# Performance work log

Measured on AMD Instinct MI355X. Metric: run time of the kernel, lower is better.

Reference implementation:

```python
import jax, jax.numpy as jnp
import numpy as np

N = 100000
E_RAND = 1600000
F_IN = 500
HID = 32
N_CLS = 40
EPS = 1e-12


def setup_inputs() -> dict:
    key = jax.random.key(0)
    k_x, k_e, k_w1, k_b1, k_w2, k_b2 = jax.random.split(key, 6)
    x = jax.random.normal(k_x, (N, F_IN), dtype=jnp.float32)
    # random edges (src, dst) + self-loops (PyG AGNNConv adds self-loops)
    er = jax.random.randint(k_e, (2, E_RAND), 0, N, dtype=jnp.int64)
    loops = jnp.broadcast_to(jnp.arange(N, dtype=jnp.int64), (2, N))
    edge_index = jnp.concatenate([er, loops], axis=1)  # [2, 1_700_000]
    W1 = jax.random.normal(k_w1, (F_IN, HID), dtype=jnp.float32) * (1.0 / np.sqrt(F_IN))
    b1 = jax.random.normal(k_b1, (HID,), dtype=jnp.float32) * 0.01
    W2 = jax.random.normal(k_w2, (HID, N_CLS), dtype=jnp.float32) * (1.0 / np.sqrt(HID))
    b2 = jax.random.normal(k_b2, (N_CLS,), dtype=jnp.float32) * 0.01
    beta2 = jnp.float32(1.0)  # learnable beta of prop2
    return {"x": x, "W1": W1, "b1": b1, "W2": W2, "b2": b2,
            "beta2": beta2, "edge_index": edge_index}


def agnn_conv(x, edge_index, beta):
    # x: [N, D]; edge_index: [2, E] with (src=j, dst=i); PyG AGNNConv semantics.
    src, dst = edge_index[0], edge_index[1]
    xn = x * jax.lax.rsqrt(jnp.sum(x * x, axis=-1, keepdims=True) + EPS)  # L2 normalize
    logits = beta * jnp.sum(xn[src] * xn[dst], axis=-1)  # [E] cosine similarity
    # segment softmax over incoming edges of each dst node (self-loops => no empty segments)
    m = jax.ops.segment_max(logits, dst, num_segments=N)
    e = jnp.exp(logits - m[dst])
    s = jax.ops.segment_sum(e, dst, num_segments=N)
    alpha = e / (s[dst] + 1e-16)  # [E]
    out = jax.ops.segment_sum(alpha[:, None] * x[src], dst, num_segments=N)  # [N, D]
    return out


def reference(x, W1, b1, W2, b2, beta2, edge_index):
    # eval mode: dropout is identity
    h = jax.nn.relu(x @ W1 + b1)                 # [N, HID]
    h = agnn_conv(h, edge_index, jnp.float32(1.0))  # prop1: fixed beta
    h = agnn_conv(h, edge_index, beta2)             # prop2: learnable beta
    return h @ W2 + b2                              # [N, N_CLS]
```

## Files before the change

### kernel.cpp

```cpp
#include <hip/hip_runtime.h>
#include <hip/hip_bf16.h>
#include <math.h>

#define F_IN 500
#define HID 32
#define NCLS 40


__global__ void hist_kernel(const int* __restrict__ dst, int E, int* __restrict__ deg) {
    int e = blockIdx.x * 256 + threadIdx.x;
    if (e < E) atomicAdd(&deg[dst[e]], 1);
}

__global__ __launch_bounds__(1024) void scan_local_kernel(const int* __restrict__ deg,
                                                          int* __restrict__ rowptr,
                                                          int* __restrict__ blocksum, int N) {
    __shared__ int wsum[16];
    int tid = threadIdx.x;
    int lane = tid & 63;
    int wid = tid >> 6;
    int idx = blockIdx.x * 1024 + tid;
    int v = (idx < N) ? deg[idx] : 0;
    int x = v;
    #pragma unroll
    for (int off = 1; off < 64; off <<= 1) {
        int y = __shfl_up(x, off);
        if (lane >= off) x += y;
    }
    if (lane == 63) wsum[wid] = x;
    __syncthreads();
    if (wid == 0 && lane < 16) {
        int wv = wsum[lane];
        #pragma unroll
        for (int off = 1; off < 16; off <<= 1) {
            int y = __shfl_up(wv, off);
            if (lane >= off) wv += y;
        }
        wsum[lane] = wv;
    }
    __syncthreads();
    int base = (wid > 0) ? wsum[wid - 1] : 0;
    if (idx < N) rowptr[idx] = base + x - v;
    if (tid == 0) blocksum[blockIdx.x] = wsum[15];
}

__global__ __launch_bounds__(128) void scan_offsets_kernel(int* __restrict__ blocksum,
                                                           int* __restrict__ rowptrN, int nb) {
    __shared__ int ws[2];
    int tid = threadIdx.x;
    int lane = tid & 63;
    int wid = tid >> 6;
    int v = (tid < nb) ? blocksum[tid] : 0;
    int x = v;
    #pragma unroll
    for (int off = 1; off < 64; off <<= 1) {
        int y = __shfl_up(x, off);
        if (lane >= off) x += y;
    }
    if (lane == 63) ws[wid] = x;
    __syncthreads();
    int base = (wid == 1) ? ws[0] : 0;
    int excl = base + x - v;
    if (tid < nb) blocksum[tid] = excl;
    if (tid == nb - 1) *rowptrN = excl + v;
}

__global__ __launch_bounds__(1024) void scan_add_kernel(const int* __restrict__ blocksum,
                                                        int* __restrict__ rowptr,
                                                        int* __restrict__ cursor, int N) {
    int idx = blockIdx.x * 1024 + threadIdx.x;
    if (idx < N) {
        int v = rowptr[idx] + blocksum[blockIdx.x];
        rowptr[idx] = v;
        cursor[idx] = v;
    }
}

__global__ void scatter_kernel(const int* __restrict__ src, const int* __restrict__ dst,
                               int E, int* __restrict__ cursor, int* __restrict__ col) {
    int e = blockIdx.x * 256 + threadIdx.x;
    if (e < E) {
        int pos = atomicAdd(&cursor[dst[e]], 1);
        col[pos] = src[e];
    }
}

__global__ __launch_bounds__(256) void gemm1_kernel(const float* __restrict__ x,
                                                    const float* __restrict__ W1,
                                                    const float* __restrict__ b1,
                                                    float* __restrict__ h1,
                                                    float* __restrict__ rn, int N) {
    __shared__ float xs[128][33];
    __shared__ float w1s[32][32];
    int tid = threadIdx.x;
    int ct = tid & 3;
    int rt = tid >> 2;
    long row0 = (long)blockIdx.x * 128;

    float acc[2][8];
    #pragma unroll
    for (int q = 0; q < 2; ++q)
        #pragma unroll
        for (int j = 0; j < 8; ++j) acc[q][j] = 0.f;

    float4 xr[4];
    float w1r[4];

    #pragma unroll
    for (int s = 0; s < 4; ++s) {
        int f4 = tid + (s << 8);
        int row = f4 >> 3;
        int c4 = (f4 & 7) << 2;
        long gr = row0 + row;
        xr[s] = make_float4(0.f, 0.f, 0.f, 0.f);
        if (gr < N && c4 < F_IN) xr[s] = *(const float4*)(x + gr * F_IN + c4);
        int idx = tid + (s << 8);
        w1r[s] = W1[(long)(idx >> 5) * 32 + (idx & 31)];
    }

    for (int kc = 0; kc < 512; kc += 32) {
        __syncthreads();
        #pragma unroll
        for (int s = 0; s < 4; ++s) {
            int f4 = tid + (s << 8);
            int row = f4 >> 3;
            int c4 = (f4 & 7) << 2;
            xs[row][c4 + 0] = xr[s].x;
            xs[row][c4 + 1] = xr[s].y;
            xs[row][c4 + 2] = xr[s].z;
            xs[row][c4 + 3] = xr[s].w;
            int idx = tid + (s << 8);
            w1s[idx >> 5][idx & 31] = w1r[s];
        }
        __syncthreads();

        int kn = kc + 32;
        if (kn < 512) {
            #pragma unroll
            for (int s = 0; s < 4; ++s) {
                int f4 = tid + (s << 8);
                int row = f4 >> 3;
                int c4 = (f4 & 7) << 2;
                long gr = row0 + row;
                int k = kn + c4;
                xr[s] = make_float4(0.f, 0.f, 0.f, 0.f);
                if (gr < N && k < F_IN) xr[s] = *(const float4*)(x + gr * F_IN + k);
                int idx = tid + (s << 8);
                int kk = kn + (idx >> 5);
                w1r[s] = (kk < F_IN) ? W1[(long)kk * 32 + (idx & 31)] : 0.f;
            }
        }

        #pragma unroll 8
        for (int kk = 0; kk < 32; ++kk) {
            float4 wa = *(const float4*)&w1s[kk][ct * 8];
            float4 wb = *(const float4*)&w1s[kk][ct * 8 + 4];
            float x0 = xs[rt * 2 + 0][kk];
            float x1 = xs[rt * 2 + 1][kk];
            acc[0][0] += x0 * wa.x; acc[0][1] += x0 * wa.y;
            acc[0][2] += x0 * wa.z; acc[0][3] += x0 * wa.w;
            acc[0][4] += x0 * wb.x; acc[0][5] += x0 * wb.y;
            acc[0][6] += x0 * wb.z; acc[0][7] += x0 * wb.w;
            acc[1][0] += x1 * wa.x; acc[1][1] += x1 * wa.y;
            acc[1][2] += x1 * wa.z; acc[1][3] += x1 * wa.w;
            acc[1][4] += x1 * wb.x; acc[1][5] += x1 * wb.y;
            acc[1][6] += x1 * wb.z; acc[1][7] += x1 * wb.w;
        }
    }

    float4 ba = *(const float4*)(b1 + ct * 8);
    float4 bb = *(const float4*)(b1 + ct * 8 + 4);
    #pragma unroll
    for (int q = 0; q < 2; ++q) {
        long gr = row0 + rt * 2 + q;
        float4 oa, ob;
        oa.x = fmaxf(acc[q][0] + ba.x, 0.f);
        oa.y = fmaxf(acc[q][1] + ba.y, 0.f);
        oa.z = fmaxf(acc[q][2] + ba.z, 0.f);
        oa.w = fmaxf(acc[q][3] + ba.w, 0.f);
        ob.x = fmaxf(acc[q][4] + bb.x, 0.f);
        ob.y = fmaxf(acc[q][5] + bb.y, 0.f);
        ob.z = fmaxf(acc[q][6] + bb.z, 0.f);
        ob.w = fmaxf(acc[q][7] + bb.w, 0.f);
        float ss = oa.x * oa.x + oa.y * oa.y + oa.z * oa.z + oa.w * oa.w
                 + ob.x * ob.x + ob.y * ob.y + ob.z * ob.z + ob.w * ob.w;
        ss += __shfl_xor(ss, 1);
        ss += __shfl_xor(ss, 2);
        if (gr < N) {
            float* op = h1 + gr * 32 + ct * 8;
            *(float4*)op = oa;
            *(float4*)(op + 4) = ob;
            if (ct == 0) rn[gr] = rsqrtf(ss + 1e-12f);
        }
    }
}

__global__ __launch_bounds__(256) void conv_kernel(const float* __restrict__ h,
                                                   const float* __restrict__ rn,
                                                   const int* __restrict__ rowptr,
                                                   const int* __restrict__ col,
                                                   const float* __restrict__ betaPtr,
                                                   float* __restrict__ out,
                                                   float* __restrict__ rnOut, int N) {
    int sub = threadIdx.x & 7;
    int i = blockIdx.x * 32 + (threadIdx.x >> 3);
    if (i >= N) return;
    float beta = betaPtr ? betaPtr[0] : 1.0f;
    float shift = fabsf(beta);
    long lsub = (long)(sub << 2);
    float4 hi = *(const float4*)(h + ((long)i << 5) + lsub);
    float bri = beta * rn[i];
    int e0 = rowptr[i];
    int e1 = rowptr[i + 1];

    float s = 0.f;
    float4 acc = make_float4(0.f, 0.f, 0.f, 0.f);
    int e = e0;
    for (; e + 4 <= e1; e += 4) {
        int j0 = col[e + 0], j1 = col[e + 1], j2 = col[e + 2], j3 = col[e + 3];
        float r0 = rn[j0], r1 = rn[j1], r2 = rn[j2], r3 = rn[j3];
        float4 v0 = *(const float4*)(h + ((long)j0 << 5) + lsub);
        float4 v1 = *(const float4*)(h + ((long)j1 << 5) + lsub);
        float4 v2 = *(const float4*)(h + ((long)j2 << 5) + lsub);
        float4 v3 = *(const float4*)(h + ((long)j3 << 5) + lsub);
        float d0 = hi.x * v0.x + hi.y * v0.y + hi.z * v0.z + hi.w * v0.w;
        float d1 = hi.x * v1.x + hi.y * v1.y + hi.z * v1.z + hi.w * v1.w;
        float d2 = hi.x * v2.x + hi.y * v2.y + hi.z * v2.z + hi.w * v2.w;
        float d3 = hi.x * v3.x + hi.y * v3.y + hi.z * v3.z + hi.w * v3.w;
        d0 += __shfl_xor(d0, 1); d1 += __shfl_xor(d1, 1);
        d2 += __shfl_xor(d2, 1); d3 += __shfl_xor(d3, 1);
        d0 += __shfl_xor(d0, 2); d1 += __shfl_xor(d1, 2);
        d2 += __shfl_xor(d2, 2); d3 += __shfl_xor(d3, 2);
        d0 += __shfl_xor(d0, 4); d1 += __shfl_xor(d1, 4);
        d2 += __shfl_xor(d2, 4); d3 += __shfl_xor(d3, 4);
        float w0 = __expf(bri * r0 * d0 - shift);
        float w1 = __expf(bri * r1 * d1 - shift);
        float w2 = __expf(bri * r2 * d2 - shift);
        float w3 = __expf(bri * r3 * d3 - shift);
        s += (w0 + w1) + (w2 + w3);
        acc.x += w0 * v0.x + w1 * v1.x + w2 * v2.x + w3 * v3.x;
        acc.y += w0 * v0.y + w1 * v1.y + w2 * v2.y + w3 * v3.y;
        acc.z += w0 * v0.z + w1 * v1.z + w2 * v2.z + w3 * v3.z;
        acc.w += w0 * v0.w + w1 * v1.w + w2 * v2.w + w3 * v3.w;
    }
    for (; e < e1; ++e) {
        int j = col[e];
        float rj = rn[j];
        float4 v = *(const float4*)(h + ((long)j << 5) + lsub);
        float d = hi.x * v.x + hi.y * v.y + hi.z * v.z + hi.w * v.w;
        d += __shfl_xor(d, 1);
        d += __shfl_xor(d, 2);
        d += __shfl_xor(d, 4);
        float w = __expf(bri * rj * d - shift);
        s += w;
        acc.x += w * v.x; acc.y += w * v.y; acc.z += w * v.z; acc.w += w * v.w;
    }

    float inv = 1.f / (s + 1e-16f);
    float4 o = make_float4(acc.x * inv, acc.y * inv, acc.z * inv, acc.w * inv);
    *(float4*)(out + ((long)i << 5) + lsub) = o;
    if (rnOut) {
        float ss = o.x * o.x + o.y * o.y + o.z * o.z + o.w * o.w;
        ss += __shfl_xor(ss, 1);
        ss += __shfl_xor(ss, 2);
        ss += __shfl_xor(ss, 4);
        if (sub == 0) rnOut[i] = rsqrtf(ss + 1e-12f);
    }
}

__global__ __launch_bounds__(256) void gemm2_kernel(const float* __restrict__ h3,
                                                    const float* __restrict__ W2,
                                                    const float* __restrict__ b2,
                                                    float* __restrict__ out, int N) {
    __shared__ float w2s[HID * NCLS];
    __shared__ float b2s[NCLS];
    for (int i = threadIdx.x; i < HID * NCLS; i += 256) w2s[i] = W2[i];
    if (threadIdx.x < NCLS) b2s[threadIdx.x] = b2[threadIdx.x];
    __syncthreads();

    int idx = blockIdx.x * 256 + threadIdx.x;
    if (idx >= N * NCLS) return;
    int n = idx / NCLS;
    int c = idx - n * NCLS;

    const float4* hp = (const float4*)(h3 + (long)n * 32);
    float acc = b2s[c];
    #pragma unroll
    for (int k4 = 0; k4 < 8; ++k4) {
        float4 hv = hp[k4];
        acc += hv.x * w2s[(k4 * 4 + 0) * NCLS + c];
        acc += hv.y * w2s[(k4 * 4 + 1) * NCLS + c];
        acc += hv.z * w2s[(k4 * 4 + 2) * NCLS + c];
        acc += hv.w * w2s[(k4 * 4 + 3) * NCLS + c];
    }
    out[idx] = acc;
}


extern "C" void kernel_launch(void* const* d_in, const int* in_sizes, int n_in,
                              void* d_out, int out_size, void* d_ws, size_t ws_size,
                              hipStream_t stream) {
    const float* x     = (const float*)d_in[0];
    const float* W1    = (const float*)d_in[1];
    const float* b1    = (const float*)d_in[2];
    const float* W2    = (const float*)d_in[3];
    const float* b2    = (const float*)d_in[4];
    const float* beta2 = (const float*)d_in[5];
    const int*   ei    = (const int*)d_in[6];

    int N = in_sizes[0] / F_IN;
    int E = in_sizes[6] / 2;
    const int* src = ei;
    const int* dst = ei + E;
    float* out = (float*)d_out;

    char* p = (char*)d_ws;
    auto alloc = [&](size_t bytes) -> void* {
        void* r = (void*)p;
        p += (bytes + 255) & ~(size_t)255;
        return r;
    };
    float* h1  = (float*)alloc((size_t)N * 32 * 4);
    float* h2  = (float*)alloc((size_t)N * 32 * 4);
    float* rn1 = (float*)alloc((size_t)N * 4);
    float* rn2 = (float*)alloc((size_t)N * 4);
    int* deg      = (int*)alloc((size_t)N * 4);
    int* rowptr   = (int*)alloc((size_t)(N + 1) * 4);
    int* cursor   = (int*)alloc((size_t)N * 4);
    int* col      = (int*)alloc((size_t)E * 4);
    int* blocksum = (int*)alloc(1024 * 4);
    float* h3   = h1;

    int eblocks = (E + 255) / 256;
    int sblocks = (N + 1023) / 1024;
    int cblocks = (N + 31) / 32;

    gemm1_kernel<<<(N + 127) / 128, 256, 0, stream>>>(x, W1, b1, h1, rn1, N);

    hipMemsetAsync(deg, 0, (size_t)N * 4, stream);
    hist_kernel<<<eblocks, 256, 0, stream>>>(dst, E, deg);
    scan_local_kernel<<<sblocks, 1024, 0, stream>>>(deg, rowptr, blocksum, N);
    scan_offsets_kernel<<<1, 128, 0, stream>>>(blocksum, rowptr + N, sblocks);
    scan_add_kernel<<<sblocks, 1024, 0, stream>>>(blocksum, rowptr, cursor, N);
    scatter_kernel<<<eblocks, 256, 0, stream>>>(src, dst, E, cursor, col);

    conv_kernel<<<cblocks, 256, 0, stream>>>(h1, rn1, rowptr, col, nullptr, h2, rn2, N);
    conv_kernel<<<cblocks, 256, 0, stream>>>(h2, rn2, rowptr, col, beta2, h3, nullptr, N);

    gemm2_kernel<<<(N * NCLS + 255) / 256, 256, 0, stream>>>(h3, W2, b2, out, N);
}
```

Measured before the change: 610.7 us.

## Build CSR via two-level bucketed counting sort with LDS staging

Replaces the per-edge global atomic histogram and scatter CSR build with a two-pass bucket sort. Edges are first binned into 256-node buckets using LDS atomics and staged contiguously in global memory. A per-bucket kernel then computes local row offsets and scatters columns using shared-memory atomics. This removes the random global atomics and scattered col writes of the old build, at the cost of an extra staging buffer and a packed src/dst-low encoding that assumes node ids fit in 17 bits and at most 512 buckets.

```diff
diff --git a/kernel.cpp b/kernel.cpp
--- a/kernel.cpp
+++ b/kernel.cpp
@@ -1,26 +1,37 @@
 #include <hip/hip_runtime.h>
-#include <hip/hip_bf16.h>
 #include <math.h>
 
 #define F_IN 500
 #define HID 32
 #define NCLS 40
 
-
-__global__ void hist_kernel(const int* __restrict__ dst, int E, int* __restrict__ deg) {
-    int e = blockIdx.x * 256 + threadIdx.x;
-    if (e < E) atomicAdd(&deg[dst[e]], 1);
-}
-
-__global__ __launch_bounds__(1024) void scan_local_kernel(const int* __restrict__ deg,
-                                                          int* __restrict__ rowptr,
-                                                          int* __restrict__ blocksum, int N) {
-    __shared__ int wsum[16];
+#define NPB 256
+#define MAXB 512
+#define EPB 16384
+
+__global__ __launch_bounds__(256) void csr_count_kernel(const int* __restrict__ dst, int E,
+                                                        int* __restrict__ gcnt, int nb) {
+    __shared__ int cnt[MAXB];
     int tid = threadIdx.x;
-    int lane = tid & 63;
-    int wid = tid >> 6;
-    int idx = blockIdx.x * 1024 + tid;
-    int v = (idx < N) ? deg[idx] : 0;
+    for (int i = tid; i < MAXB; i += 256) cnt[i] = 0;
+    __syncthreads();
+    long e0 = (long)blockIdx.x * EPB;
+    #pragma unroll 4
+    for (int k = 0; k < EPB / 256; ++k) {
+        long e = e0 + tid + k * 256;
+        if (e < E) atomicAdd(&cnt[dst[e] >> 8], 1);
+    }
+    __syncthreads();
+    for (int b = tid; b < nb; b += 256)
+        if (cnt[b]) atomicAdd(&gcnt[b], cnt[b]);
+}
+
+__global__ __launch_bounds__(512) void csr_bscan_kernel(const int* __restrict__ gcnt,
+                                                        int* __restrict__ bucketptr,
+                                                        int* __restrict__ bcur, int nb) {
+    __shared__ int wsum[8];
+    int tid = threadIdx.x, lane = tid & 63, wid = tid >> 6;
+    int v = (tid < nb) ? gcnt[tid] : 0;
     int x = v;
     #pragma unroll
     for (int off = 1; off < 64; off <<= 1) {
@@ -29,60 +40,120 @@
     }
     if (lane == 63) wsum[wid] = x;
     __syncthreads();
-    if (wid == 0 && lane < 16) {
+    if (wid == 0 && lane < 8) {
         int wv = wsum[lane];
         #pragma unroll
-        for (int off = 1; off < 16; off <<= 1) {
+        for (int off = 1; off < 8; off <<= 1) {
             int y = __shfl_up(wv, off);
             if (lane >= off) wv += y;
         }
         wsum[lane] = wv;
     }
     __syncthreads();
-    int base = (wid > 0) ? wsum[wid - 1] : 0;
-    if (idx < N) rowptr[idx] = base + x - v;
-    if (tid == 0) blocksum[blockIdx.x] = wsum[15];
-}
-
-__global__ __launch_bounds__(128) void scan_offsets_kernel(int* __restrict__ blocksum,
-                                                           int* __restrict__ rowptrN, int nb) {
-    __shared__ int ws[2];
-    int tid = threadIdx.x;
-    int lane = tid & 63;
-    int wid = tid >> 6;
-    int v = (tid < nb) ? blocksum[tid] : 0;
+    int excl = ((wid > 0) ? wsum[wid - 1] : 0) + x - v;
+    if (tid < nb) { bucketptr[tid] = excl; bcur[tid] = excl; }
+    if (tid == nb - 1) bucketptr[nb] = excl + v;
+}
+
+__global__ __launch_bounds__(512) void csr_bin_kernel(const int* __restrict__ src,
+                                                      const int* __restrict__ dst, int E,
+                                                      int* __restrict__ bcur,
+                                                      int* __restrict__ gstage, int nb) {
+    __shared__ int cnt[MAXB], off[MAXB], cur[MAXB], gbase[MAXB];
+    __shared__ int stage[EPB];
+    __shared__ int wsum[8];
+    int tid = threadIdx.x, lane = tid & 63, wid = tid >> 6;
+    cnt[tid] = 0;
+    __syncthreads();
+    long e0 = (long)blockIdx.x * EPB;
+    #pragma unroll 4
+    for (int k = 0; k < EPB / 512; ++k) {
+        long e = e0 + tid + k * 512;
+        if (e < E) atomicAdd(&cnt[dst[e] >> 8], 1);
+    }
+    __syncthreads();
+    int v = cnt[tid];
     int x = v;
     #pragma unroll
-    for (int off = 1; off < 64; off <<= 1) {
-        int y = __shfl_up(x, off);
-        if (lane >= off) x += y;
-    }
-    if (lane == 63) ws[wid] = x;
-    __syncthreads();
-    int base = (wid == 1) ? ws[0] : 0;
-    int excl = base + x - v;
-    if (tid < nb) blocksum[tid] = excl;
-    if (tid == nb - 1) *rowptrN = excl + v;
-}
-
-__global__ __launch_bounds__(1024) void scan_add_kernel(const int* __restrict__ blocksum,
-                                                        int* __restrict__ rowptr,
-                                                        int* __restrict__ cursor, int N) {
-    int idx = blockIdx.x * 1024 + threadIdx.x;
-    if (idx < N) {
-        int v = rowptr[idx] + blocksum[blockIdx.x];
-        rowptr[idx] = v;
-        cursor[idx] = v;
-    }
-}
-
-__global__ void scatter_kernel(const int* __restrict__ src, const int* __restrict__ dst,
-                               int E, int* __restrict__ cursor, int* __restrict__ col) {
-    int e = blockIdx.x * 256 + threadIdx.x;
-    if (e < E) {
-        int pos = atomicAdd(&cursor[dst[e]], 1);
-        col[pos] = src[e];
-    }
+    for (int o = 1; o < 64; o <<= 1) {
+        int y = __shfl_up(x, o);
+        if (lane >= o) x += y;
+    }
+    if (lane == 63) wsum[wid] = x;
+    __syncthreads();
+    if (wid == 0 && lane < 8) {
+        int wv = wsum[lane];
+        #pragma unroll
+        for (int o = 1; o < 8; o <<= 1) {
+            int y = __shfl_up(wv, o);
+            if (lane >= o) wv += y;
+        }
+        wsum[lane] = wv;
+    }
+    __syncthreads();
+    int excl = ((wid > 0) ? wsum[wid - 1] : 0) + x - v;
+    off[tid] = excl;
+    cur[tid] = excl;
+    if (v) gbase[tid] = atomicAdd(&bcur[tid], v);
+    __syncthreads();
+    #pragma unroll 4
+    for (int k = 0; k < EPB / 512; ++k) {
+        long e = e0 + tid + k * 512;
+        if (e < E) {
+            int dd = dst[e];
+            int b = dd >> 8;
+            int w = src[e] | ((dd & 255) << 17);
+            int p = atomicAdd(&cur[b], 1);
+            stage[p] = w;
+        }
+    }
+    __syncthreads();
+    for (int b = wid; b < nb; b += 8) {
+        int c = cnt[b];
+        int lo = off[b], go = gbase[b];
+        for (int k = lane; k < c; k += 64) gstage[go + k] = stage[lo + k];
+    }
+}
+
+__global__ __launch_bounds__(256) void csr_scatter_kernel(const int* __restrict__ bucketptr,
+                                                          const int* __restrict__ gstage,
+                                                          int* __restrict__ rowptr,
+                                                          int* __restrict__ col, int N, int nb) {
+    __shared__ int cur[NPB];
+    __shared__ int wsum[4];
+    int tid = threadIdx.x, lane = tid & 63, wid = tid >> 6;
+    int b = blockIdx.x;
+    int node0 = b << 8;
+    int ebase = bucketptr[b], eend = bucketptr[b + 1];
+    cur[tid] = 0;
+    __syncthreads();
+    for (int e = ebase + tid; e < eend; e += 256)
+        atomicAdd(&cur[((unsigned)gstage[e]) >> 17], 1);
+    __syncthreads();
+    int v = cur[tid];
+    int x = v;
+    #pragma unroll
+    for (int o = 1; o < 64; o <<= 1) {
+        int y = __shfl_up(x, o);
+        if (lane >= o) x += y;
+    }
+    if (lane == 63) wsum[wid] = x;
+    __syncthreads();
+    if (tid == 0) {
+        int a0 = wsum[0], a1 = wsum[1], a2 = wsum[2];
+        wsum[0] = 0; wsum[1] = a0; wsum[2] = a0 + a1; wsum[3] = a0 + a1 + a2;
+    }
+    __syncthreads();
+    int start = ebase + wsum[wid] + x - v;
+    if (node0 + tid < N) rowptr[node0 + tid] = start;
+    cur[tid] = start;
+    __syncthreads();
+    for (int e = ebase + tid; e < eend; e += 256) {
+        unsigned w = (unsigned)gstage[e];
+        int p = atomicAdd(&cur[w >> 17], 1);
+        col[p] = (int)(w & 0x1FFFFu);
+    }
+    if (b == nb - 1 && tid == 0) rowptr[N] = eend;
 }
 
 __global__ __launch_bounds__(256) void gemm1_kernel(const float* __restrict__ x,
@@ -324,25 +395,25 @@
     float* h2  = (float*)alloc((size_t)N * 32 * 4);
     float* rn1 = (float*)alloc((size_t)N * 4);
     float* rn2 = (float*)alloc((size_t)N * 4);
-    int* deg      = (int*)alloc((size_t)N * 4);
-    int* rowptr   = (int*)alloc((size_t)(N + 1) * 4);
-    int* cursor   = (int*)alloc((size_t)N * 4);
-    int* col      = (int*)alloc((size_t)E * 4);
-    int* blocksum = (int*)alloc(1024 * 4);
-    float* h3   = h1;
-
-    int eblocks = (E + 255) / 256;
-    int sblocks = (N + 1023) / 1024;
+    int* rowptr    = (int*)alloc((size_t)(N + 1) * 4);
+    int* col       = (int*)alloc((size_t)E * 4);
+    int* gstage    = (int*)alloc((size_t)E * 4);
+    int* gcnt      = (int*)alloc((size_t)MAXB * 4);
+    int* bucketptr = (int*)alloc((size_t)(MAXB + 1) * 4);
+    int* bcur      = (int*)alloc((size_t)MAXB * 4);
+    float* h3 = h1;
+
+    int nb = (N + NPB - 1) / NPB;
+    int p1blocks = (int)(((long)E + EPB - 1) / EPB);
     int cblocks = (N + 31) / 32;
 
     gemm1_kernel<<<(N + 127) / 128, 256, 0, stream>>>(x, W1, b1, h1, rn1, N);
 
-    hipMemsetAsync(deg, 0, (size_t)N * 4, stream);
-    hist_kernel<<<eblocks, 256, 0, stream>>>(dst, E, deg);
-    scan_local_kernel<<<sblocks, 1024, 0, stream>>>(deg, rowptr, blocksum, N);
-    scan_offsets_kernel<<<1, 128, 0, stream>>>(blocksum, rowptr + N, sblocks);
-    scan_add_kernel<<<sblocks, 1024, 0, stream>>>(blocksum, rowptr, cursor, N);
-    scatter_kernel<<<eblocks, 256, 0, stream>>>(src, dst, E, cursor, col);
+    hipMemsetAsync(gcnt, 0, (size_t)nb * 4, stream);
+    csr_count_kernel<<<p1blocks, 256, 0, stream>>>(dst, E, gcnt, nb);
+    csr_bscan_kernel<<<1, 512, 0, stream>>>(gcnt, bucketptr, bcur, nb);
+    csr_bin_kernel<<<p1blocks, 512, 0, stream>>>(src, dst, E, bcur, gstage, nb);
+    csr_scatter_kernel<<<nb, 256, 0, stream>>>(bucketptr, gstage, rowptr, col, N, nb);
 
     conv_kernel<<<cblocks, 256, 0, stream>>>(h1, rn1, rowptr, col, nullptr, h2, rn2, N);
     conv_kernel<<<cblocks, 256, 0, stream>>>(h2, rn2, rowptr, col, beta2, h3, nullptr, N);
```

Measured after the change: 503.4 us. 17.6% less time.
